# Performance work log

Measured on AMD Instinct MI355X. Metric: run time of the kernel, lower is better.

Reference implementation:

```python
import jax, jax.numpy as jnp
import numpy as np

HIDDEN = 2048
N_HEADS = 16
HEAD_DIM = HIDDEN // N_HEADS  # 128
GROUP_SIZE = 128
ROPE_THETA = 10000.0
EPS = 1e-8
THRESH = 0.5


def ternary_quantize_groupwise(w):
    O, I = w.shape
    wg = w.reshape(O, I // GROUP_SIZE, GROUP_SIZE)
    scale = jnp.maximum(jnp.mean(jnp.abs(wg), axis=-1, keepdims=True), EPS)
    wn = wg / scale
    q = jnp.where(wn > THRESH, 1.0, jnp.where(wn < -THRESH, -1.0, 0.0))
    return (q * scale).reshape(O, I)


def quantize_with_ste(w):
    wq = ternary_quantize_groupwise(w)
    return w + jax.lax.stop_gradient(wq - w)


def rope_tables(seqlen):
    half = HEAD_DIM // 2
    inv_freq = 1.0 / (ROPE_THETA ** (jnp.arange(half, dtype=jnp.float32) / half))
    freqs = jnp.arange(seqlen, dtype=jnp.float32)[:, None] * inv_freq[None, :]  # [S, half]
    return jnp.cos(freqs), jnp.sin(freqs)


def apply_rope(x, cos, sin):
    # x: [B, H, S, D]; cos/sin: [S, D/2]
    d = x.shape[-1]
    x1, x2 = x[..., : d // 2], x[..., d // 2:]
    c = cos[None, None, :, :].astype(x.dtype)
    s = sin[None, None, :, :].astype(x.dtype)
    return jnp.concatenate([x1 * c - x2 * s, x1 * s + x2 * c], axis=-1)


def setup_inputs() -> dict:
    key = jax.random.key(0)
    ks = jax.random.split(key, 5)
    B, S = 1, 2048
    hidden_states = jax.random.normal(ks[0], (B, S, HIDDEN), dtype=jnp.float32)
    attention_mask = jnp.ones((B, S), dtype=jnp.int32)
    init_scale = 1.0 / np.sqrt(HIDDEN)
    wq = jax.random.normal(ks[1], (HIDDEN, HIDDEN), dtype=jnp.float32) * init_scale
    wk = jax.random.normal(ks[2], (HIDDEN, HIDDEN), dtype=jnp.float32) * init_scale
    wv = jax.random.normal(ks[3], (HIDDEN, HIDDEN), dtype=jnp.float32) * init_scale
    wo = jax.random.normal(ks[4], (HIDDEN, HIDDEN), dtype=jnp.float32) * init_scale
    return {"hidden_states": hidden_states, "attention_mask": attention_mask,
            "wq": wq, "wk": wk, "wv": wv, "wo": wo}


def reference(hidden_states, attention_mask, wq, wk, wv, wo):
    B, S, _ = hidden_states.shape
    cos, sin = rope_tables(S)

    def proj(x, w):
        w_q = quantize_with_ste(w)
        y = jnp.einsum('bsi,oi->bso', x, w_q)
        return y.reshape(B, S, N_HEADS, HEAD_DIM).transpose(0, 2, 1, 3)  # [B,H,S,D]

    q = apply_rope(proj(hidden_states, wq), cos, sin)
    k = apply_rope(proj(hidden_states, wk), cos, sin)
    v = proj(hidden_states, wv)

    scores = jnp.einsum('bhsd,bhtd->bhst', q, k) / np.sqrt(HEAD_DIM)
    causal = jnp.triu(jnp.ones((S, S), dtype=bool), k=1)
    scores = jnp.where(causal[None, None, :, :], -jnp.inf, scores)
    pad = (attention_mask == 0)[:, None, None, :]
    scores = jnp.where(pad, -jnp.inf, scores)

    probs = jax.nn.softmax(scores, axis=-1)
    out = jnp.einsum('bhst,bhtd->bhsd', probs, v)
    out = out.transpose(0, 2, 1, 3).reshape(B, S, HIDDEN)

    wo_q = quantize_with_ste(wo)
    return jnp.einsum('bso,po->bsp', out, wo_q)
```

## Files before the change

### kernel.cpp

```cpp
#include <hip/hip_runtime.h>
#include <cstdint>
#include <cstddef>


typedef __attribute__((ext_vector_type(8))) short bf16x8;
typedef __attribute__((ext_vector_type(4))) float f32x4;
typedef __attribute__((address_space(3))) void lds_void;
typedef const __attribute__((address_space(1))) void gmem_void;

__device__ __forceinline__ short f2bf(float x) {
    union { float f; uint32_t u; } c; c.f = x;
    uint32_t r = (c.u + 0x7FFFu + ((c.u >> 16) & 1u)) >> 16;
    return (short)r;
}
__device__ __forceinline__ float bf2f(short x) {
    union { uint32_t u; float f; } c; c.u = ((uint32_t)(uint16_t)x) << 16;
    return c.f;
}

__global__ __launch_bounds__(64) void zero_flag(int* f) {
    if (threadIdx.x == 0) *f = 0;
}

__global__ __launch_bounds__(256) void detect_kernel(
    const unsigned short* __restrict__ p, int n, int* __restrict__ flag)
{
    int tid = blockIdx.x * 256 + threadIdx.x;
    int cnt = 0;
    for (int i = tid; i < n; i += 65536) {
        int e = (p[i] >> 7) & 0xFF;
        cnt += (e >= 0xF0) ? 1 : 0;
    }
#pragma unroll
    for (int off = 1; off < 64; off <<= 1) cnt += __shfl_xor(cnt, off);
    if ((threadIdx.x & 63) == 0 && cnt) atomicAdd(flag, cnt);
}

__global__ __launch_bounds__(256) void convert_kernel(
    const void* __restrict__ in, short* __restrict__ out, int n,
    const int* __restrict__ flag)
{
    bool isf32 = (*flag > 1000);
    int i = (blockIdx.x * 256 + threadIdx.x) * 4;
    if (i >= n) return;
    if (isf32) {
        float4 v = *(const float4*)((const float*)in + i);
        short4 o;
        o.x = f2bf(v.x); o.y = f2bf(v.y); o.z = f2bf(v.z); o.w = f2bf(v.w);
        *(short4*)(out + i) = o;
    } else {
        *(short4*)(out + i) = *(const short4*)((const short*)in + i);
    }
}

__global__ __launch_bounds__(256) void quant_kernel(
    const void* __restrict__ w0, const void* __restrict__ w1,
    const void* __restrict__ w2, const void* __restrict__ w3,
    short* __restrict__ q0, short* __restrict__ q1,
    short* __restrict__ q2, short* __restrict__ q3,
    const int* __restrict__ flag)
{
    bool isf32 = (*flag > 1000);
    int gw   = blockIdx.x * 4 + (threadIdx.x >> 6);
    int lane = threadIdx.x & 63;
    int mat  = gw >> 15;
    int g    = gw & 32767;
    const void* w = (mat == 0) ? w0 : (mat == 1) ? w1 : (mat == 2) ? w2 : w3;
    short*      q = (mat == 0) ? q0 : (mat == 1) ? q1 : (mat == 2) ? q2 : q3;
    int idx = g * 64 + lane;
    float a, b;
    if (isf32) {
        const float* wf = (const float*)w;
        a = wf[idx * 2]; b = wf[idx * 2 + 1];
    } else {
        int pr = ((const int*)w)[idx];
        a = bf2f((short)(pr & 0xFFFF));
        b = bf2f((short)(((uint32_t)pr) >> 16));
    }
    float s = fabsf(a) + fabsf(b);
#pragma unroll
    for (int off = 1; off < 64; off <<= 1) s += __shfl_xor(s, off);
    float scale = fmaxf(s * (1.0f / 128.0f), 1e-8f);
    float na = a / scale, nb = b / scale;
    float ra = (na > 0.5f) ? scale : (na < -0.5f) ? -scale : 0.0f;
    float rb = (nb > 0.5f) ? scale : (nb < -0.5f) ? -scale : 0.0f;
    ((int*)q)[idx] = (int)(uint16_t)f2bf(ra) | ((int)(uint16_t)f2bf(rb) << 16);
}

__global__ __launch_bounds__(256) void gemm_qkv(
    const short* __restrict__ A, const short* __restrict__ B,
    short* __restrict__ Cqk, short* __restrict__ Cv)
{
    int bx = blockIdx.x, by = blockIdx.y;
    const short* Ab = A + (long long)by * 128 * 2048;
    const short* Bb = B + (long long)bx * 128 * 2048;
    __shared__ short ls[16384];
    short* lA = ls;
    short* lB = ls + 8192;
    int tid = threadIdx.x;
    int lane = tid & 63, wv = tid >> 6;
    f32x4 acc[4][4];
#pragma unroll
    for (int i = 0; i < 4; i++)
#pragma unroll
        for (int j = 0; j < 4; j++)
#pragma unroll
            for (int r = 0; r < 4; r++) acc[i][j][r] = 0.0f;

    int rbase = (wv >> 1) * 64, cbase = (wv & 1) * 64;

    for (int k0 = 0; k0 < 2048; k0 += 64) {
        __syncthreads();
#pragma unroll
        for (int i = 0; i < 4; i++) {
            int ci  = i * 256 + tid;
            int row = ci >> 3;
            int kcG = (ci & 7) ^ (row & 7);
            const short* gp = Ab + (long long)row * 2048 + k0 + kcG * 8;
            __builtin_amdgcn_global_load_lds((gmem_void*)gp, (lds_void*)(lA + ci * 8), 16, 0, 0);
        }
#pragma unroll
        for (int i = 0; i < 4; i++) {
            int ci  = i * 256 + tid;
            int row = ci >> 3;
            int kcG = (ci & 7) ^ (row & 7);
            const short* gp = Bb + (long long)row * 2048 + k0 + kcG * 8;
            __builtin_amdgcn_global_load_lds((gmem_void*)gp, (lds_void*)(lB + ci * 8), 16, 0, 0);
        }
        __syncthreads();
#pragma unroll
        for (int kk = 0; kk < 2; kk++) {
            int kc = kk * 4 + (lane >> 4);
            bf16x8 a[4], b[4];
#pragma unroll
            for (int t = 0; t < 4; t++) {
                int r = rbase + t * 16 + (lane & 15);
                a[t] = *(const bf16x8*)(lA + (r * 8 + (kc ^ (r & 7))) * 8);
            }
#pragma unroll
            for (int t = 0; t < 4; t++) {
                int r = cbase + t * 16 + (lane & 15);
                b[t] = *(const bf16x8*)(lB + (r * 8 + (kc ^ (r & 7))) * 8);
            }
#pragma unroll
            for (int mt = 0; mt < 4; mt++)
#pragma unroll
                for (int nt = 0; nt < 4; nt++)
                    acc[mt][nt] = __builtin_amdgcn_mfma_f32_16x16x32_bf16(a[mt], b[nt], acc[mt][nt], 0, 0, 0);
        }
    }

    int rq = (lane >> 4) * 4, cq = lane & 15;
    if (bx < 32) {
#pragma unroll
        for (int mt = 0; mt < 4; mt++)
#pragma unroll
            for (int nt = 0; nt < 4; nt++)
#pragma unroll
                for (int r = 0; r < 4; r++) {
                    int row = by * 128 + rbase + mt * 16 + rq + r;
                    int col = bx * 128 + cbase + nt * 16 + cq;
                    Cqk[(long long)row * 4096 + col] = f2bf(acc[mt][nt][r]);
                }
    } else {
        __syncthreads();
#pragma unroll
        for (int mt = 0; mt < 4; mt++)
#pragma unroll
            for (int nt = 0; nt < 4; nt++)
#pragma unroll
                for (int r = 0; r < 4; r++) {
                    int row = rbase + mt * 16 + rq + r;
                    int col = cbase + nt * 16 + cq;
                    int rcs = (row >> 3) ^ (col & 15);
                    ls[col * 128 + rcs * 8 + (row & 7)] = f2bf(acc[mt][nt][r]);
                }
        __syncthreads();
        int o = tid >> 1, half = tid & 1;
        long long og = (long long)((bx - 32) * 128 + o) * 2048 + by * 128;
#pragma unroll
        for (int c = 0; c < 8; c++) {
            int ch = half * 8 + c;
            int chs = ch ^ (o & 15);
            bf16x8 v = *(const bf16x8*)(ls + o * 128 + chs * 8);
            *(bf16x8*)(Cv + og + ch * 8) = v;
        }
    }
}

__global__ __launch_bounds__(256) void gemm_wo(
    const short* __restrict__ A, const short* __restrict__ B,
    float* __restrict__ C)
{
    int bx = blockIdx.x, by = blockIdx.y;
    const short* Ab = A + (long long)by * 128 * 2048;
    const short* Bb = B + (long long)bx * 64 * 2048;
    __shared__ short lA[128 * 64];
    __shared__ short lB[64 * 64];
    int tid = threadIdx.x;
    int lane = tid & 63, wv = tid >> 6;
    f32x4 acc[2][4];
#pragma unroll
    for (int i = 0; i < 2; i++)
#pragma unroll
        for (int j = 0; j < 4; j++)
#pragma unroll
            for (int r = 0; r < 4; r++) acc[i][j][r] = 0.0f;

    int rbase = wv * 32;

    for (int k0 = 0; k0 < 2048; k0 += 64) {
        __syncthreads();
#pragma unroll
        for (int i = 0; i < 4; i++) {
            int ci  = i * 256 + tid;
            int row = ci >> 3;
            int kcG = (ci & 7) ^ (row & 7);
            const short* gp = Ab + (long long)row * 2048 + k0 + kcG * 8;
            __builtin_amdgcn_global_load_lds((gmem_void*)gp, (lds_void*)(lA + ci * 8), 16, 0, 0);
        }
#pragma unroll
        for (int i = 0; i < 2; i++) {
            int ci  = i * 256 + tid;
            int row = ci >> 3;
            int kcG = (ci & 7) ^ (row & 7);
            const short* gp = Bb + (long long)row * 2048 + k0 + kcG * 8;
            __builtin_amdgcn_global_load_lds((gmem_void*)gp, (lds_void*)(lB + ci * 8), 16, 0, 0);
        }
        __syncthreads();
#pragma unroll
        for (int kk = 0; kk < 2; kk++) {
            int kc = kk * 4 + (lane >> 4);
            bf16x8 a[2], b[4];
#pragma unroll
            for (int t = 0; t < 2; t++) {
                int r = rbase + t * 16 + (lane & 15);
                a[t] = *(const bf16x8*)(lA + (r * 8 + (kc ^ (r & 7))) * 8);
            }
#pragma unroll
            for (int t = 0; t < 4; t++) {
                int r = t * 16 + (lane & 15);
                b[t] = *(const bf16x8*)(lB + (r * 8 + (kc ^ (r & 7))) * 8);
            }
#pragma unroll
            for (int mt = 0; mt < 2; mt++)
#pragma unroll
                for (int nt = 0; nt < 4; nt++)
                    acc[mt][nt] = __builtin_amdgcn_mfma_f32_16x16x32_bf16(a[mt], b[nt], acc[mt][nt], 0, 0, 0);
        }
    }

    int rq = (lane >> 4) * 4, cq = lane & 15;
#pragma unroll
    for (int mt = 0; mt < 2; mt++)
#pragma unroll
        for (int nt = 0; nt < 4; nt++)
#pragma unroll
            for (int r = 0; r < 4; r++) {
                int row = by * 128 + rbase + mt * 16 + rq + r;
                int col = bx * 64 + nt * 16 + cq;
                C[(long long)row * 2048 + col] = acc[mt][nt][r];
            }
}

__global__ __launch_bounds__(256) void rope_kernel(
    const short* __restrict__ qk,
    short* __restrict__ qr, short* __restrict__ kr)
{
    int idx = blockIdx.x * 256 + threadIdx.x;
    int d = idx & 63;
    int h = (idx >> 6) & 15;
    int s = idx >> 10;
    float inv = exp2f((float)d * -0.20762050593261719f);
    float ang = (float)s * inv;
    float sn, c;
    sincosf(ang, &sn, &c);
    long long io = (long long)s * 4096 + h * 128 + d;
    long long oo = (long long)h * 262144 + (long long)s * 128 + d;
    float x1 = bf2f(qk[io]), x2 = bf2f(qk[io + 64]);
    qr[oo]      = f2bf(x1 * c - x2 * sn);
    qr[oo + 64] = f2bf(x1 * sn + x2 * c);
    x1 = bf2f(qk[io + 2048]); x2 = bf2f(qk[io + 2112]);
    kr[oo]      = f2bf(x1 * c - x2 * sn);
    kr[oo + 64] = f2bf(x1 * sn + x2 * c);
}

__global__ __launch_bounds__(256) void flash_kernel(
    const short* __restrict__ q_r, const short* __restrict__ k_r,
    const short* __restrict__ v_t, float* __restrict__ Opart,
    float* __restrict__ mpart, float* __restrict__ lpart)
{
    const float SC = 0.08838834764831845f;
    int bid = blockIdx.x;
    int qt = 31 - (bid >> 5);
    int h  = (bid >> 1) & 15;
    int z  = bid & 1;
    int n  = qt + 1;
    int jhalf = (n + 1) >> 1;
    int jb = z ? jhalf : 0;
    int je = z ? n : jhalf;

    int tid = threadIdx.x, lane = tid & 63, wv = tid >> 6;
    int quad = lane >> 4, lm = lane & 15;

    __shared__ short lK[64 * 128];
    __shared__ short lV[128 * 64];
    __shared__ short lP[64 * 64];

    const short* qb = q_r + h * 262144 + (qt * 64 + wv * 16) * 128;
    const short* kb = k_r + h * 262144;
    const short* vb = v_t + h * 128 * 2048;

    bf16x8 aq[4];
#pragma unroll
    for (int kc = 0; kc < 4; kc++)
        aq[kc] = *(const bf16x8*)(qb + lm * 128 + kc * 32 + quad * 8);

    f32x4 ao[8];
#pragma unroll
    for (int nt = 0; nt < 8; nt++)
#pragma unroll
        for (int r = 0; r < 4; r++) ao[nt][r] = 0.0f;
    float mrow[4], lrow[4];
#pragma unroll
    for (int r = 0; r < 4; r++) { mrow[r] = -1e30f; lrow[r] = 0.0f; }

    if (jb < je) {
#pragma unroll
        for (int i = 0; i < 4; i++) {
            int ci = i * 256 + tid;
            int r = ci >> 4, cp = ci & 15;
            int c = (cp & 8) | ((cp & 7) ^ (r & 7));
            const short* gp = kb + (jb * 64 + r) * 128 + c * 8;
            __builtin_amdgcn_global_load_lds((gmem_void*)gp, (lds_void*)(lK + ci * 8), 16, 0, 0);
        }
    }
    __syncthreads();

    for (int jt = jb; jt < je; jt++) {
#pragma unroll
        for (int i = 0; i < 4; i++) {
            int ci = i * 256 + tid;
            int r = ci >> 3, cp = ci & 7;
            int c = cp ^ (r & 7);
            const short* gp = vb + r * 2048 + jt * 64 + c * 8;
            __builtin_amdgcn_global_load_lds((gmem_void*)gp, (lds_void*)(lV + ci * 8), 16, 0, 0);
        }
        f32x4 as[4];
#pragma unroll
        for (int nt = 0; nt < 4; nt++)
#pragma unroll
            for (int r = 0; r < 4; r++) as[nt][r] = 0.0f;
#pragma unroll
        for (int kc = 0; kc < 4; kc++) {
#pragma unroll
            for (int nt = 0; nt < 4; nt++) {
                int r = nt * 16 + lm;
                int c = kc * 4 + quad;
                int slot = (c & 8) | ((c & 7) ^ (r & 7));
                bf16x8 bk = *(const bf16x8*)(lK + (r * 16 + slot) * 8);
                as[nt] = __builtin_amdgcn_mfma_f32_16x16x32_bf16(aq[kc], bk, as[nt], 0, 0, 0);
            }
        }
        bool diag = (jt == qt);
#pragma unroll
        for (int nt = 0; nt < 4; nt++)
#pragma unroll
            for (int r = 0; r < 4; r++) {
                float s = as[nt][r] * SC;
                if (diag) {
                    int qg = wv * 16 + quad * 4 + r;
                    int tg = nt * 16 + lm;
                    if (tg > qg) s = -1e30f;
                }
                as[nt][r] = s;
            }
#pragma unroll
        for (int r = 0; r < 4; r++) {
            float mx = fmaxf(fmaxf(as[0][r], as[1][r]), fmaxf(as[2][r], as[3][r]));
#pragma unroll
            for (int off = 1; off < 16; off <<= 1) mx = fmaxf(mx, __shfl_xor(mx, off));
            float mnew = fmaxf(mrow[r], mx);
            float alpha = __expf(mrow[r] - mnew);
            mrow[r] = mnew;
            float psum = 0.0f;
#pragma unroll
            for (int nt = 0; nt < 4; nt++) {
                float p = __expf(as[nt][r] - mnew);
                as[nt][r] = p;
                psum += p;
            }
#pragma unroll
            for (int off = 1; off < 16; off <<= 1) psum += __shfl_xor(psum, off);
            lrow[r] = lrow[r] * alpha + psum;
#pragma unroll
            for (int nt = 0; nt < 8; nt++) ao[nt][r] *= alpha;
            int row = wv * 16 + quad * 4 + r;
#pragma unroll
            for (int nt = 0; nt < 4; nt++) {
                int slot = (nt * 2 + (lm >> 3) + 2 * quad) & 7;
                lP[row * 64 + slot * 8 + (lm & 7)] = f2bf(as[nt][r]);
            }
        }
        __syncthreads();
        if (jt + 1 < je) {
#pragma unroll
            for (int i = 0; i < 4; i++) {
                int ci = i * 256 + tid;
                int r = ci >> 4, cp = ci & 15;
                int c = (cp & 8) | ((cp & 7) ^ (r & 7));
                const short* gp = kb + ((jt + 1) * 64 + r) * 128 + c * 8;
                __builtin_amdgcn_global_load_lds((gmem_void*)gp, (lds_void*)(lK + ci * 8), 16, 0, 0);
            }
        }
#pragma unroll
        for (int kt = 0; kt < 2; kt++) {
            int prow = wv * 16 + lm;
            int slot = (kt * 4 + quad + 2 * (lm >> 2)) & 7;
            bf16x8 ap = *(const bf16x8*)(lP + prow * 64 + slot * 8);
#pragma unroll
            for (int nt = 0; nt < 8; nt++) {
                int r = nt * 16 + lm;
                int c = kt * 4 + quad;
                int vslot = c ^ (r & 7);
                bf16x8 bv = *(const bf16x8*)(lV + (r * 8 + vslot) * 8);
                ao[nt] = __builtin_amdgcn_mfma_f32_16x16x32_bf16(ap, bv, ao[nt], 0, 0, 0);
            }
        }
        __syncthreads();
    }
    float* Ob = Opart + (long long)z * 4194304;
#pragma unroll
    for (int r = 0; r < 4; r++) {
        int sg = qt * 64 + wv * 16 + quad * 4 + r;
#pragma unroll
        for (int nt = 0; nt < 8; nt++) {
            int dg = h * 128 + nt * 16 + lm;
            Ob[(long long)sg * 2048 + dg] = ao[nt][r];
        }
        if (lm == 0) {
            mpart[z * 32768 + h * 2048 + sg] = mrow[r];
            lpart[z * 32768 + h * 2048 + sg] = lrow[r];
        }
    }
}

__global__ __launch_bounds__(256) void combine_kernel(
    const float* __restrict__ O0, const float* __restrict__ O1,
    const float* __restrict__ mpart, const float* __restrict__ lpart,
    short* __restrict__ attn)
{
    int idx = blockIdx.x * 256 + threadIdx.x;
    int e = idx * 4;
    int s = e >> 11, h = (e & 2047) >> 7;
    float m0 = mpart[h * 2048 + s], m1 = mpart[32768 + h * 2048 + s];
    float l0 = lpart[h * 2048 + s], l1 = lpart[32768 + h * 2048 + s];
    float M = fmaxf(m0, m1);
    float w0 = __expf(m0 - M), w1 = __expf(m1 - M);
    float inv = 1.0f / (l0 * w0 + l1 * w1);
    float4 a = *(const float4*)(O0 + e);
    float4 b = *(const float4*)(O1 + e);
    short4 o;
    o.x = f2bf((a.x * w0 + b.x * w1) * inv);
    o.y = f2bf((a.y * w0 + b.y * w1) * inv);
    o.z = f2bf((a.z * w0 + b.z * w1) * inv);
    o.w = f2bf((a.w * w0 + b.w * w1) * inv);
    *(short4*)(attn + e) = o;
}

extern "C" void kernel_launch(void* const* d_in, const int* in_sizes, int n_in,
                              void* d_out, int out_size, void* d_ws, size_t ws_size,
                              hipStream_t stream)
{
    const void* x  = d_in[0];
    const void* wq = d_in[2];
    const void* wk = d_in[3];
    const void* wv = d_in[4];
    const void* wo = d_in[5];

    char* ws = (char*)d_ws;
    size_t off = 0;
    auto alloc = [&](size_t b) { void* p = ws + off; off += (b + 255) & ~(size_t)255; return p; };
    short* wqkv_q = (short*)alloc(25165824);
    short* wo_q   = (short*)alloc(8388608);
    short* qk     = (short*)alloc(16777216);
    short* v_t    = (short*)alloc(8388608);
    short* q_r    = (short*)alloc(8388608);
    short* k_r    = (short*)alloc(8388608);
    short* attn   = (short*)alloc(8388608);
    short* x_bf   = (short*)alloc(8388608);
    float* Opart  = (float*)alloc(33554432);
    float* mpart  = (float*)alloc(262144);
    float* lpart  = (float*)alloc(262144);
    int*   flag   = (int*)alloc(256);
    if (off > ws_size) return;

    zero_flag<<<1, 64, 0, stream>>>(flag);
    detect_kernel<<<256, 256, 0, stream>>>(
        (const unsigned short*)x, in_sizes[0], flag);
    convert_kernel<<<4096, 256, 0, stream>>>(x, x_bf, 4194304, flag);

    quant_kernel<<<32768, 256, 0, stream>>>(wq, wk, wv, wo,
        wqkv_q, wqkv_q + 4194304, wqkv_q + 8388608, wo_q, flag);

    gemm_qkv<<<dim3(48,16), 256, 0, stream>>>(x_bf, wqkv_q, qk, v_t);

    rope_kernel<<<8192, 256, 0, stream>>>(qk, q_r, k_r);

    flash_kernel<<<1024, 256, 0, stream>>>(q_r, k_r, v_t, Opart, mpart, lpart);
    combine_kernel<<<4096, 256, 0, stream>>>(
        Opart, Opart + 4194304, mpart, lpart, attn);

    gemm_wo<<<dim3(32,16), 256, 0, stream>>>(attn, wo_q, (float*)d_out);
}
```

Baseline: 331.5 us.

## Rewrite QKV GEMM with 256x256 tiles, double-buffered LDS and separate V transpose

The QKV projection GEMM moves from 128x128 tiles with 4 waves to 256x256 tiles with 8 waves. It double-buffers the LDS stages so the next K-slice prefetch overlaps the MFMA work, raises MFMA priority with s_setprio, and remaps workgroups into a swizzled order for cache locality. The fused V-transpose epilogue is split out into a separate vtrans_kernel, and the qkv intermediate now aliases the Opart buffer. This cuts global re-reads per output and hides load latency, at the cost of one extra launch, higher register pressure from 32 accumulators, and only 192 workgroups.

Result: faster. 320.2 us (-3.4%).

```diff
diff --git a/kernel.cpp b/kernel.cpp
--- a/kernel.cpp
+++ b/kernel.cpp
@@ -87,104 +87,136 @@
     ((int*)q)[idx] = (int)(uint16_t)f2bf(ra) | ((int)(uint16_t)f2bf(rb) << 16);
 }
 
-__global__ __launch_bounds__(256) void gemm_qkv(
+__global__ __launch_bounds__(512, 2) void gemm_qkv(
     const short* __restrict__ A, const short* __restrict__ B,
-    short* __restrict__ Cqk, short* __restrict__ Cv)
-{
-    int bx = blockIdx.x, by = blockIdx.y;
-    const short* Ab = A + (long long)by * 128 * 2048;
-    const short* Bb = B + (long long)bx * 128 * 2048;
-    __shared__ short ls[16384];
-    short* lA = ls;
-    short* lB = ls + 8192;
+    short* __restrict__ C)
+{
+    __shared__ short lds[32768];
+    short* A0 = lds;          short* A1 = lds + 8192;
+    short* B0 = lds + 16384;  short* B1 = lds + 24576;
+
+    int wg = blockIdx.y * 24 + blockIdx.x;
+    int sw = (wg & 7) * 24 + (wg >> 3);
+    int bx = sw % 24, by = sw / 24;
+
+    const short* Ab = A + (long long)by * 256 * 2048;
+    const short* Bb = B + (long long)bx * 256 * 2048;
+
+    int tid = threadIdx.x, lane = tid & 63, wid = tid >> 6;
+    int wr = wid >> 2, wc = wid & 3;
+    int quad = lane >> 4, lm = lane & 15;
+
+    f32x4 acc[8][4];
+#pragma unroll
+    for (int i = 0; i < 8; i++)
+#pragma unroll
+        for (int j = 0; j < 4; j++)
+#pragma unroll
+            for (int r = 0; r < 4; r++) acc[i][j][r] = 0.0f;
+
+    auto stage = [&](int tn, short* dA, short* dB) {
+#pragma unroll
+        for (int l = 0; l < 2; l++) {
+            int ci = l * 512 + tid;
+            int R = ci >> 2;
+            int kc = ((ci & 3) - (R >> 1)) & 3;
+            const short* gp = Ab + (long long)R * 2048 + tn * 32 + kc * 8;
+            __builtin_amdgcn_global_load_lds((gmem_void*)gp, (lds_void*)(dA + ci * 8), 16, 0, 0);
+        }
+#pragma unroll
+        for (int l = 0; l < 2; l++) {
+            int ci = l * 512 + tid;
+            int R = ci >> 2;
+            int kc = ((ci & 3) - (R >> 1)) & 3;
+            const short* gp = Bb + (long long)R * 2048 + tn * 32 + kc * 8;
+            __builtin_amdgcn_global_load_lds((gmem_void*)gp, (lds_void*)(dB + ci * 8), 16, 0, 0);
+        }
+    };
+
+    auto tile = [&](short* cA, short* cB, short* nA, short* nB, int tn, bool pf) {
+        if (pf) stage(tn, nA, nB);
+        bf16x8 af[4], bg[4];
+#pragma unroll
+        for (int m = 0; m < 4; m++) {
+            int R = wr * 128 + m * 16 + lm;
+            af[m] = *(const bf16x8*)(cA + R * 32 + (((quad + (R >> 1)) & 3) << 3));
+        }
+#pragma unroll
+        for (int n = 0; n < 4; n++) {
+            int R = wc * 64 + n * 16 + lm;
+            bg[n] = *(const bf16x8*)(cB + R * 32 + (((quad + (R >> 1)) & 3) << 3));
+        }
+        __builtin_amdgcn_s_barrier();
+        __builtin_amdgcn_s_setprio(1);
+#pragma unroll
+        for (int m = 0; m < 4; m++)
+#pragma unroll
+            for (int n = 0; n < 4; n++)
+                acc[m][n] = __builtin_amdgcn_mfma_f32_16x16x32_bf16(af[m], bg[n], acc[m][n], 0, 0, 0);
+        __builtin_amdgcn_s_setprio(0);
+        __builtin_amdgcn_s_barrier();
+#pragma unroll
+        for (int m = 0; m < 4; m++) {
+            int R = wr * 128 + 64 + m * 16 + lm;
+            af[m] = *(const bf16x8*)(cA + R * 32 + (((quad + (R >> 1)) & 3) << 3));
+        }
+        __builtin_amdgcn_s_barrier();
+        __builtin_amdgcn_s_setprio(1);
+#pragma unroll
+        for (int m = 0; m < 4; m++)
+#pragma unroll
+            for (int n = 0; n < 4; n++)
+                acc[m + 4][n] = __builtin_amdgcn_mfma_f32_16x16x32_bf16(af[m], bg[n], acc[m + 4][n], 0, 0, 0);
+        __builtin_amdgcn_s_setprio(0);
+        if (pf) asm volatile("s_waitcnt vmcnt(0)" ::: "memory");
+        __builtin_amdgcn_s_barrier();
+    };
+
+    stage(0, A0, B0);
+    asm volatile("s_waitcnt vmcnt(0)" ::: "memory");
+    __syncthreads();
+
+    for (int t = 0; t < 64; t += 2) {
+        tile(A0, B0, A1, B1, t + 1, true);
+        tile(A1, B1, A0, B0, t + 2, t + 2 < 64);
+    }
+
+#pragma unroll
+    for (int m = 0; m < 8; m++)
+#pragma unroll
+        for (int n = 0; n < 4; n++)
+#pragma unroll
+            for (int r = 0; r < 4; r++) {
+                int row = by * 256 + wr * 128 + m * 16 + quad * 4 + r;
+                int col = bx * 256 + wc * 64 + n * 16 + lm;
+                C[(long long)row * 6144 + col] = f2bf(acc[m][n][r]);
+            }
+}
+
+__global__ __launch_bounds__(256) void vtrans_kernel(
+    const short* __restrict__ qkv, short* __restrict__ v_t)
+{
+    __shared__ short lt[4096];
+    int bt = blockIdx.x, bo = blockIdx.y;
     int tid = threadIdx.x;
-    int lane = tid & 63, wv = tid >> 6;
-    f32x4 acc[4][4];
-#pragma unroll
-    for (int i = 0; i < 4; i++)
-#pragma unroll
-        for (int j = 0; j < 4; j++)
-#pragma unroll
-            for (int r = 0; r < 4; r++) acc[i][j][r] = 0.0f;
-
-    int rbase = (wv >> 1) * 64, cbase = (wv & 1) * 64;
-
-    for (int k0 = 0; k0 < 2048; k0 += 64) {
-        __syncthreads();
-#pragma unroll
-        for (int i = 0; i < 4; i++) {
-            int ci  = i * 256 + tid;
-            int row = ci >> 3;
-            int kcG = (ci & 7) ^ (row & 7);
-            const short* gp = Ab + (long long)row * 2048 + k0 + kcG * 8;
-            __builtin_amdgcn_global_load_lds((gmem_void*)gp, (lds_void*)(lA + ci * 8), 16, 0, 0);
-        }
-#pragma unroll
-        for (int i = 0; i < 4; i++) {
-            int ci  = i * 256 + tid;
-            int row = ci >> 3;
-            int kcG = (ci & 7) ^ (row & 7);
-            const short* gp = Bb + (long long)row * 2048 + k0 + kcG * 8;
-            __builtin_amdgcn_global_load_lds((gmem_void*)gp, (lds_void*)(lB + ci * 8), 16, 0, 0);
-        }
-        __syncthreads();
-#pragma unroll
-        for (int kk = 0; kk < 2; kk++) {
-            int kc = kk * 4 + (lane >> 4);
-            bf16x8 a[4], b[4];
-#pragma unroll
-            for (int t = 0; t < 4; t++) {
-                int r = rbase + t * 16 + (lane & 15);
-                a[t] = *(const bf16x8*)(lA + (r * 8 + (kc ^ (r & 7))) * 8);
-            }
-#pragma unroll
-            for (int t = 0; t < 4; t++) {
-                int r = cbase + t * 16 + (lane & 15);
-                b[t] = *(const bf16x8*)(lB + (r * 8 + (kc ^ (r & 7))) * 8);
-            }
-#pragma unroll
-            for (int mt = 0; mt < 4; mt++)
-#pragma unroll
-                for (int nt = 0; nt < 4; nt++)
-                    acc[mt][nt] = __builtin_amdgcn_mfma_f32_16x16x32_bf16(a[mt], b[nt], acc[mt][nt], 0, 0, 0);
-        }
-    }
-
-    int rq = (lane >> 4) * 4, cq = lane & 15;
-    if (bx < 32) {
-#pragma unroll
-        for (int mt = 0; mt < 4; mt++)
-#pragma unroll
-            for (int nt = 0; nt < 4; nt++)
-#pragma unroll
-                for (int r = 0; r < 4; r++) {
-                    int row = by * 128 + rbase + mt * 16 + rq + r;
-                    int col = bx * 128 + cbase + nt * 16 + cq;
-                    Cqk[(long long)row * 4096 + col] = f2bf(acc[mt][nt][r]);
-                }
-    } else {
-        __syncthreads();
-#pragma unroll
-        for (int mt = 0; mt < 4; mt++)
-#pragma unroll
-            for (int nt = 0; nt < 4; nt++)
-#pragma unroll
-                for (int r = 0; r < 4; r++) {
-                    int row = rbase + mt * 16 + rq + r;
-                    int col = cbase + nt * 16 + cq;
-                    int rcs = (row >> 3) ^ (col & 15);
-                    ls[col * 128 + rcs * 8 + (row & 7)] = f2bf(acc[mt][nt][r]);
-                }
-        __syncthreads();
-        int o = tid >> 1, half = tid & 1;
-        long long og = (long long)((bx - 32) * 128 + o) * 2048 + by * 128;
-#pragma unroll
-        for (int c = 0; c < 8; c++) {
-            int ch = half * 8 + c;
-            int chs = ch ^ (o & 15);
-            bf16x8 v = *(const bf16x8*)(ls + o * 128 + chs * 8);
-            *(bf16x8*)(Cv + og + ch * 8) = v;
-        }
+    int r = tid >> 3, c = tid & 7;
+#pragma unroll
+    for (int h = 0; h < 2; h++) {
+        int row = h * 32 + r;
+        bf16x8 v = *(const bf16x8*)(qkv + (long long)(bt * 64 + row) * 6144 + 4096 + bo * 64 + c * 8);
+        *(bf16x8*)(lt + row * 64 + ((c ^ (row & 7)) << 3)) = v;
+    }
+    __syncthreads();
+#pragma unroll
+    for (int h = 0; h < 2; h++) {
+        int o = h * 32 + r;
+        bf16x8 ov;
+#pragma unroll
+        for (int k = 0; k < 8; k++) {
+            int row = c * 8 + k;
+            ov[k] = lt[row * 64 + ((((o >> 3) ^ (row & 7))) << 3) + (o & 7)];
+        }
+        *(bf16x8*)(v_t + (long long)(bo * 64 + o) * 2048 + bt * 64 + c * 8) = ov;
     }
 }
 
@@ -275,7 +307,7 @@
     float ang = (float)s * inv;
     float sn, c;
     sincosf(ang, &sn, &c);
-    long long io = (long long)s * 4096 + h * 128 + d;
+    long long io = (long long)s * 6144 + h * 128 + d;
     long long oo = (long long)h * 262144 + (long long)s * 128 + d;
     float x1 = bf2f(qk[io]), x2 = bf2f(qk[io + 64]);
     qr[oo]      = f2bf(x1 * c - x2 * sn);
@@ -483,13 +515,13 @@
     auto alloc = [&](size_t b) { void* p = ws + off; off += (b + 255) & ~(size_t)255; return p; };
     short* wqkv_q = (short*)alloc(25165824);
     short* wo_q   = (short*)alloc(8388608);
-    short* qk     = (short*)alloc(16777216);
+    float* Opart  = (float*)alloc(33554432);
+    short* qkv    = (short*)Opart;
     short* v_t    = (short*)alloc(8388608);
     short* q_r    = (short*)alloc(8388608);
     short* k_r    = (short*)alloc(8388608);
     short* attn   = (short*)alloc(8388608);
     short* x_bf   = (short*)alloc(8388608);
-    float* Opart  = (float*)alloc(33554432);
     float* mpart  = (float*)alloc(262144);
     float* lpart  = (float*)alloc(262144);
     int*   flag   = (int*)alloc(256);
@@ -503,13 +535,14 @@
     quant_kernel<<<32768, 256, 0, stream>>>(wq, wk, wv, wo,
         wqkv_q, wqkv_q + 4194304, wqkv_q + 8388608, wo_q, flag);
 
-    gemm_qkv<<<dim3(48,16), 256, 0, stream>>>(x_bf, wqkv_q, qk, v_t);
-
-    rope_kernel<<<8192, 256, 0, stream>>>(qk, q_r, k_r);
+    gemm_qkv<<<dim3(24, 8), 512, 0, stream>>>(x_bf, wqkv_q, qkv);
+
+    rope_kernel<<<8192, 256, 0, stream>>>(qkv, q_r, k_r);
+    vtrans_kernel<<<dim3(32, 32), 256, 0, stream>>>(qkv, v_t);
 
     flash_kernel<<<1024, 256, 0, stream>>>(q_r, k_r, v_t, Opart, mpart, lpart);
     combine_kernel<<<4096, 256, 0, stream>>>(
         Opart, Opart + 4194304, mpart, lpart, attn);
 
-    gemm_wo<<<dim3(32,16), 256, 0, stream>>>(attn, wo_q, (float*)d_out);
-}
+    gemm_wo<<<dim3(32, 16), 256, 0, stream>>>(attn, wo_q, (float*)d_out);
+}
```
